# Performance work log

Measured on AMD Instinct MI355X. Metric: run time of the kernel, lower is better.

## Reference

```python
import jax, jax.numpy as jnp
import numpy as np

D_MODEL = 768
NUM_HEADS = 12
DEPTH = D_MODEL // NUM_HEADS
LN_EPS = 1e-5


def setup_inputs() -> dict:
    key = jax.random.key(0)
    ks = jax.random.split(key, 5)
    B, S = 2, 2048
    scale = 1.0 / np.sqrt(D_MODEL)
    return {
        "Q": jax.random.normal(ks[0], (B, S, D_MODEL), jnp.float32),
        "W_q": jax.random.normal(ks[1], (D_MODEL, D_MODEL), jnp.float32) * scale,
        "b_q": jnp.zeros((D_MODEL,), jnp.float32),
        "W_k": jax.random.normal(ks[2], (D_MODEL, D_MODEL), jnp.float32) * scale,
        "b_k": jnp.zeros((D_MODEL,), jnp.float32),
        "W_v": jax.random.normal(ks[3], (D_MODEL, D_MODEL), jnp.float32) * scale,
        "b_v": jnp.zeros((D_MODEL,), jnp.float32),
        "W_o": jax.random.normal(ks[4], (D_MODEL, D_MODEL), jnp.float32) * scale,
        "b_o": jnp.zeros((D_MODEL,), jnp.float32),
        "ln_gamma": jnp.ones((D_MODEL,), jnp.float32),
        "ln_beta": jnp.zeros((D_MODEL,), jnp.float32),
    }


def _split_heads(x, B):
    # [B, S, D] -> [B, H, S, depth]
    return x.reshape(B, -1, NUM_HEADS, DEPTH).transpose(0, 2, 1, 3)


def reference(Q, W_q, b_q, W_k, b_k, W_v, b_v, W_o, b_o, ln_gamma, ln_beta):
    B = Q.shape[0]
    residual = Q
    # torch Linear: x @ W.T + b
    q = _split_heads(Q @ W_q.T + b_q, B)  # [B,H,S,dh]
    k = _split_heads(Q @ W_k.T + b_k, B)
    v = _split_heads(Q @ W_v.T + b_v, B)
    scores = jnp.einsum("bhqd,bhkd->bhqk", q, k) / jnp.sqrt(jnp.float32(DEPTH))
    attn = jax.nn.softmax(scores, axis=-1)
    out = jnp.einsum("bhqk,bhkd->bhqd", attn, v)
    out = out.transpose(0, 2, 1, 3).reshape(B, -1, D_MODEL)
    out = out @ W_o.T + b_o
    x = out + residual
    mu = jnp.mean(x, axis=-1, keepdims=True)
    var = jnp.mean(jnp.square(x - mu), axis=-1, keepdims=True)
    return (x - mu) * jax.lax.rsqrt(var + LN_EPS) * ln_gamma + ln_beta
```

## Files before the change

### kernel.cpp

```cpp
#include <hip/hip_runtime.h>
#include <hip/hip_bf16.h>

#define D_MODEL 768
#define S_LEN   2048
#define BATCH   2
#define NHEAD   12
#define DH      64
#define NTOK    (BATCH * S_LEN)
#define NBH     (BATCH * NHEAD)

typedef __attribute__((ext_vector_type(8))) short bf16x8;
typedef __attribute__((ext_vector_type(4))) float f32x4;

__device__ inline unsigned short f2bf(float f) {
    union { float f; unsigned u; } v; v.f = f;
    unsigned u = v.u;
    u += 0x7fffu + ((u >> 16) & 1u);
    return (unsigned short)(u >> 16);
}

__device__ inline unsigned pack_bf2(float a, float b) {
    union { __hip_bfloat162 h2; unsigned u; } cv;
    cv.h2 = __float22bfloat162_rn(make_float2(a, b));
    return cv.u;
}

__device__ inline float bf2f(unsigned short u) {
    union { unsigned u; float f; } c; c.u = ((unsigned)u) << 16; return c.f;
}

__device__ inline void stage16(const void* g, void* l) {
    __builtin_amdgcn_global_load_lds(
        (const __attribute__((address_space(1))) unsigned*)g,
        (__attribute__((address_space(3))) unsigned*)l, 16, 0, 0);
}

__global__ __launch_bounds__(256) void convert_kernel(
    const float* __restrict__ Q,
    const float* __restrict__ Wq, const float* __restrict__ Wk,
    const float* __restrict__ Wv, const float* __restrict__ Wo,
    unsigned short* __restrict__ Xb,
    unsigned short* __restrict__ Wqb, unsigned short* __restrict__ Wkb,
    unsigned short* __restrict__ Wvb, unsigned short* __restrict__ Wob)
{
    const int XV = NTOK * D_MODEL / 4;
    const int WV = D_MODEL * D_MODEL / 4;
    int idx = blockIdx.x * 256 + threadIdx.x;
    if (idx >= XV + 4 * WV) return;

    const float* src; unsigned short* dst; int off;
    if (idx < XV) { src = Q; dst = Xb; off = idx; }
    else {
        int i2 = idx - XV;
        int seg = i2 / WV; off = i2 - seg * WV;
        if      (seg == 0) { src = Wq; dst = Wqb; }
        else if (seg == 1) { src = Wk; dst = Wkb; }
        else if (seg == 2) { src = Wv; dst = Wvb; }
        else               { src = Wo; dst = Wob; }
    }
    float4 v = reinterpret_cast<const float4*>(src)[off];
    uint2 o;
    o.x = pack_bf2(v.x, v.y);
    o.y = pack_bf2(v.z, v.w);
    reinterpret_cast<uint2*>(dst)[off] = o;
}

#define STAGE_TILE(glob, rowstrideB, row0, k0, ldsbase, nIss)                 \
    _Pragma("unroll")                                                          \
    for (int i = 0; i < (nIss); ++i) {                                         \
        int L = i * 4096 + wv * 1024 + lane * 16;                              \
        int row = L >> 7;                                                      \
        int colb = (L & 127) ^ ((row & 7) << 4);                               \
        stage16((const char*)(glob) + (size_t)((row0) + row) * (rowstrideB)    \
                    + ((k0) << 1) + colb,                                      \
                (char*)(ldsbase) + i * 4096 + wv * 1024);                      \
    }

__global__ __launch_bounds__(256) void qkv_gemm_kernel(
    const unsigned short* __restrict__ Xb,
    const unsigned short* __restrict__ Wall,
    const float* __restrict__ bq, const float* __restrict__ bk,
    const float* __restrict__ bv,
    unsigned short* __restrict__ qb, unsigned short* __restrict__ kb,
    unsigned short* __restrict__ vtb)
{
    const int lane = threadIdx.x & 63;
    const int wv   = threadIdx.x >> 6;
    const int lr   = lane & 15;
    const int lg   = lane >> 4;
    const int wr   = wv >> 1;
    const int wc   = wv & 1;
    const int row0g = blockIdx.y * 128;
    const int col0g = blockIdx.x * 128;

    __shared__ __align__(16) unsigned short At[2][128 * 64];
    __shared__ __align__(16) unsigned short Bt[2][128 * 64];

    f32x4 acc[4][4] = {};

    STAGE_TILE(Xb,   1536, row0g, 0, At[0], 4);
    STAGE_TILE(Wall, 1536, col0g, 0, Bt[0], 4);
    __syncthreads();

    for (int s = 0; s < 12; ++s) {
        int cur = s & 1;
        if (s < 11) {
            STAGE_TILE(Xb,   1536, row0g, (s + 1) * 64, At[cur ^ 1], 4);
            STAGE_TILE(Wall, 1536, col0g, (s + 1) * 64, Bt[cur ^ 1], 4);
        }
        bf16x8 a[4][2], b[4][2];
#pragma unroll
        for (int mm = 0; mm < 4; ++mm) {
            int row = wr * 64 + mm * 16 + lr, sw = (row & 7) << 4;
#pragma unroll
            for (int ks = 0; ks < 2; ++ks)
                a[mm][ks] = *reinterpret_cast<const bf16x8*>(
                    (const char*)At[cur] + row * 128 + ((ks * 64 + lg * 16) ^ sw));
        }
#pragma unroll
        for (int n = 0; n < 4; ++n) {
            int row = wc * 64 + n * 16 + lr, sw = (row & 7) << 4;
#pragma unroll
            for (int ks = 0; ks < 2; ++ks)
                b[n][ks] = *reinterpret_cast<const bf16x8*>(
                    (const char*)Bt[cur] + row * 128 + ((ks * 64 + lg * 16) ^ sw));
        }
#pragma unroll
        for (int ks = 0; ks < 2; ++ks)
#pragma unroll
            for (int mm = 0; mm < 4; ++mm)
#pragma unroll
                for (int n = 0; n < 4; ++n)
                    acc[mm][n] = __builtin_amdgcn_mfma_f32_16x16x32_bf16(
                        a[mm][ks], b[n][ks], acc[mm][n], 0, 0, 0);
        __syncthreads();
    }

    const int which   = blockIdx.x / 6;
    const int colbase = (blockIdx.x % 6) * 128;
    const float* bias = (which == 0) ? bq : (which == 1) ? bk : bv;
#pragma unroll
    for (int mm = 0; mm < 4; ++mm) {
#pragma unroll
        for (int n = 0; n < 4; ++n) {
            int col = colbase + wc * 64 + n * 16 + lr;
            float bval = bias[col];
            int h = col >> 6, d = col & 63;
            int rowg = row0g + wr * 64 + mm * 16 + lg * 4;
            int bb = rowg >> 11, s0 = rowg & 2047;
            if (which == 2) {
                uint2 w;
                w.x = pack_bf2(acc[mm][n][0] + bval, acc[mm][n][1] + bval);
                w.y = pack_bf2(acc[mm][n][2] + bval, acc[mm][n][3] + bval);
                *reinterpret_cast<uint2*>(
                    vtb + ((size_t)(bb * NHEAD + h) * DH + d) * S_LEN + s0) = w;
            } else {
                unsigned short* dst = (which == 0) ? qb : kb;
#pragma unroll
                for (int r = 0; r < 4; ++r)
                    dst[((size_t)(bb * NHEAD + h) * S_LEN + s0 + r) * DH + d] =
                        f2bf(acc[mm][n][r] + bval);
            }
        }
    }
}

#define SMPV(BUF, S, M, L, ACC, BPTR)                                          \
    {                                                                          \
        float g0 = fmaxf(fmaxf(S[0][0], S[0][1]), S[0][2]);                    \
        float g1 = fmaxf(fmaxf(S[0][3], S[1][0]), S[1][1]);                    \
        float g2 = fmaxf(fmaxf(S[1][2], S[1][3]), S[2][0]);                    \
        float g3 = fmaxf(fmaxf(S[2][1], S[2][2]), S[2][3]);                    \
        float g4 = fmaxf(fmaxf(S[3][0], S[3][1]), S[3][2]);                    \
        float mx = fmaxf(fmaxf(fmaxf(g0, g1), g2), fmaxf(fmaxf(g3, g4), S[3][3])); \
        if (__any(mx * SC > M + 8.0f)) {                                       \
            float mg = mx * SC;                                                \
            mg = fmaxf(mg, __shfl_xor(mg, 16));                                \
            mg = fmaxf(mg, __shfl_xor(mg, 32));                                \
            float mn = fmaxf(M, mg);                                           \
            float sf = __builtin_amdgcn_exp2f(M - mn);                         \
            M = mn; L *= sf;                                                   \
            _Pragma("unroll")                                                  \
            for (int t = 0; t < 4; ++t) ACC[t] *= sf;                          \
        }                                                                      \
        float p[16];                                                           \
        _Pragma("unroll")                                                      \
        for (int kt = 0; kt < 4; ++kt)                                         \
            _Pragma("unroll")                                                  \
            for (int r = 0; r < 4; ++r)                                        \
                p[kt * 4 + r] = __builtin_amdgcn_exp2f(fmaf(S[kt][r], SC, -M)); \
        float sum = ((p[0] + p[1]) + (p[2] + p[3])) + ((p[4] + p[5]) + (p[6] + p[7])); \
        sum += ((p[8] + p[9]) + (p[10] + p[11])) + ((p[12] + p[13]) + (p[14] + p[15])); \
        L += sum;                                                              \
        _Pragma("unroll")                                                      \
        for (int kt = 0; kt < 4; ++kt) {                                       \
            uint2 w;                                                           \
            w.x = pack_bf2(p[kt * 4 + 0], p[kt * 4 + 1]);                      \
            w.y = pack_bf2(p[kt * 4 + 2], p[kt * 4 + 3]);                      \
            *(uint2*)(plw + kt * 32 + lg * 8) = w;                             \
        }                                                                      \
        union { bf16x8 v; uint2 u[2]; } bp0, bp1;                              \
        bp0.u[0] = *(const uint2*)(plr);                                       \
        bp0.u[1] = *(const uint2*)(plr + 8);                                   \
        bp1.u[0] = *(const uint2*)(plr + 64);                                  \
        bp1.u[1] = *(const uint2*)(plr + 72);                                  \
        __builtin_amdgcn_s_setprio(1);                                         \
        _Pragma("unroll")                                                      \
        for (int t = 0; t < 4; ++t) {                                          \
            bf16x8 av0 = *(const bf16x8*)(rdV[BUF] + t * 2048);                \
            bf16x8 av1 = *(const bf16x8*)(rdV[BUF] + t * 2048 + oD);           \
            ACC[t] = __builtin_amdgcn_mfma_f32_16x16x32_bf16(av0, bp0.v, ACC[t], 0, 0, 0); \
            ACC[t] = __builtin_amdgcn_mfma_f32_16x16x32_bf16(av1, bp1.v, ACC[t], 0, 0, 0); \
        }                                                                      \
        __builtin_amdgcn_s_setprio(0);                                         \
    }

#define AC(BUF, DOSTAGE, VM)                                                   \
    {                                                                          \
        if (DOSTAGE) {                                                         \
            stage16(kg, sdK[((BUF) + 2) % 3]); kg += 8192;                     \
            stage16(vg, sdV[((BUF) + 2) % 3]); vg += 128;                      \
        }                                                                      \
        f32x4 sA[4] = {}, sB[4] = {};                                          \
        __builtin_amdgcn_s_setprio(1);                                         \
        _Pragma("unroll")                                                      \
        for (int kt = 0; kt < 4; ++kt) {                                       \
            bf16x8 ak0 = *(const bf16x8*)(rdK[BUF] + kt * 2048);               \
            bf16x8 ak1 = *(const bf16x8*)(rdK[BUF] + kt * 2048 + oD);          \
            sA[kt] = __builtin_amdgcn_mfma_f32_16x16x32_bf16(ak0, bqA0, sA[kt], 0, 0, 0); \
            sB[kt] = __builtin_amdgcn_mfma_f32_16x16x32_bf16(ak0, bqB0, sB[kt], 0, 0, 0); \
            sA[kt] = __builtin_amdgcn_mfma_f32_16x16x32_bf16(ak1, bqA1, sA[kt], 0, 0, 0); \
            sB[kt] = __builtin_amdgcn_mfma_f32_16x16x32_bf16(ak1, bqB1, sB[kt], 0, 0, 0); \
        }                                                                      \
        __builtin_amdgcn_s_setprio(0);                                         \
        SMPV(BUF, sA, mA, lA, accA, plr)                                       \
        SMPV(BUF, sB, mB, lB, accB, plr)                                       \
        if ((VM) == 2) {                                                       \
            asm volatile("s_waitcnt vmcnt(2)" ::: "memory");                   \
            __builtin_amdgcn_s_barrier();                                      \
        } else if ((VM) == 0) {                                                \
            asm volatile("s_waitcnt vmcnt(0)" ::: "memory");                   \
            __builtin_amdgcn_s_barrier();                                      \
        }                                                                      \
    }

template<int KS>
__global__ __launch_bounds__(512) void attn_kernel(
    const unsigned short* __restrict__ qb, const unsigned short* __restrict__ kb,
    const unsigned short* __restrict__ vtb,
    unsigned short* __restrict__ attnb,
    unsigned short* __restrict__ Opart,
    float2* __restrict__ mlbuf)
{
    const int lane = threadIdx.x & 63;
    const int wv   = threadIdx.x >> 6;
    const int lr   = lane & 15;
    const int lg   = lane >> 4;
    const int bh   = blockIdx.y;
    const int h    = bh % NHEAD, bb = bh / NHEAD;
    const int q0   = blockIdx.x * 256 + wv * 32;
    const int ks   = (KS == 2) ? blockIdx.z : 0;

    __shared__ __align__(16) unsigned short Kt[3][4096];
    __shared__ __align__(16) unsigned short Vt[3][4096];
    __shared__ __align__(16) unsigned short PL[8][16][68];

    const char* kbase = (const char*)(kb  + (size_t)bh * S_LEN * DH)
                        + (size_t)ks * (S_LEN / KS) * 128;
    const char* vbase = (const char*)(vtb + (size_t)bh * DH * S_LEN)
                        + (size_t)ks * (S_LEN / KS) * 2;
    const unsigned short* qptr = qb + ((size_t)bh * S_LEN + q0) * DH;

    bf16x8 bqA0 = *reinterpret_cast<const bf16x8*>(qptr + (size_t)lr * DH + lg * 8);
    bf16x8 bqA1 = *reinterpret_cast<const bf16x8*>(qptr + (size_t)lr * DH + 32 + lg * 8);
    bf16x8 bqB0 = *reinterpret_cast<const bf16x8*>(qptr + (size_t)(16 + lr) * DH + lg * 8);
    bf16x8 bqB1 = *reinterpret_cast<const bf16x8*>(qptr + (size_t)(16 + lr) * DH + 32 + lg * 8);

    const int swr = (lr & 7) << 4;
    const int o0  = (lg * 16) ^ swr;
    const int oD  = (o0 ^ 64) - o0;
    const int L1  = wv * 1024 + lane * 16;
    const int r1  = L1 >> 7;
    const int cb1 = (L1 & 127) ^ ((r1 & 7) << 4);

    const char* kg = kbase + (size_t)r1 * 128 + cb1;
    const char* vg = vbase + (size_t)r1 * 4096 + cb1;
    char* sdK[3] = { (char*)Kt[0] + wv * 1024, (char*)Kt[1] + wv * 1024,
                     (char*)Kt[2] + wv * 1024 };
    char* sdV[3] = { (char*)Vt[0] + wv * 1024, (char*)Vt[1] + wv * 1024,
                     (char*)Vt[2] + wv * 1024 };
    const char* rdK[3] = {
        (const char*)Kt[0] + lr * 128 + o0,
        (const char*)Kt[1] + lr * 128 + o0,
        (const char*)Kt[2] + lr * 128 + o0 };
    const char* rdV[3] = {
        (const char*)Vt[0] + lr * 128 + o0,
        (const char*)Vt[1] + lr * 128 + o0,
        (const char*)Vt[2] + lr * 128 + o0 };
    char* plw = (char*)PL + wv * 2176 + lr * 136;
    const char* plr = plw + lg * 16;

    float mA = -1e30f, lA = 0.f, mB = -1e30f, lB = 0.f;
    f32x4 accA[4] = {}, accB[4] = {};
    const float SC = 0.125f * 1.44269504088896f;

    stage16(kg, sdK[0]); kg += 8192;
    stage16(vg, sdV[0]); vg += 128;
    stage16(kg, sdK[1]); kg += 8192;
    stage16(vg, sdV[1]); vg += 128;
    asm volatile("s_waitcnt vmcnt(2)" ::: "memory");
    __builtin_amdgcn_s_barrier();

    if constexpr (KS == 2) {
        for (int it = 0; it < 4; ++it) {
            AC(0, 1, 2); AC(1, 1, 2); AC(2, 1, 2);
        }
        AC(0, 1, 2);
        AC(1, 1, 2);
        AC(2, 0, 0);
        AC(0, 0, -1);
    } else {
        for (int it = 0; it < 10; ++it) {
            AC(0, 1, 2); AC(1, 1, 2); AC(2, 1, 2);
        }
        AC(0, 0, 0);
        AC(1, 0, -1);
    }

    lA += __shfl_xor(lA, 16); lA += __shfl_xor(lA, 32);
    lB += __shfl_xor(lB, 16); lB += __shfl_xor(lB, 32);

    if constexpr (KS == 1) {
        float rlA = 1.0f / lA, rlB = 1.0f / lB;
        size_t rbA = ((size_t)(bb * S_LEN + q0 + lr)) * D_MODEL + h * DH;
        size_t rbB = ((size_t)(bb * S_LEN + q0 + 16 + lr)) * D_MODEL + h * DH;
#pragma unroll
        for (int t = 0; t < 4; ++t) {
            *reinterpret_cast<unsigned*>(attnb + rbA + t * 16 + lg * 4) =
                pack_bf2(accA[t][0] * rlA, accA[t][1] * rlA);
            *reinterpret_cast<unsigned*>(attnb + rbA + t * 16 + lg * 4 + 2) =
                pack_bf2(accA[t][2] * rlA, accA[t][3] * rlA);
            *reinterpret_cast<unsigned*>(attnb + rbB + t * 16 + lg * 4) =
                pack_bf2(accB[t][0] * rlB, accB[t][1] * rlB);
            *reinterpret_cast<unsigned*>(attnb + rbB + t * 16 + lg * 4 + 2) =
                pack_bf2(accB[t][2] * rlB, accB[t][3] * rlB);
        }
    } else {
        size_t baseA = ((size_t)(ks * NBH + bh) * S_LEN + q0 + lr) * 64;
        size_t baseB = ((size_t)(ks * NBH + bh) * S_LEN + q0 + 16 + lr) * 64;
#pragma unroll
        for (int t = 0; t < 4; ++t) {
            *reinterpret_cast<unsigned*>(Opart + baseA + t * 16 + lg * 4) =
                pack_bf2(accA[t][0], accA[t][1]);
            *reinterpret_cast<unsigned*>(Opart + baseA + t * 16 + lg * 4 + 2) =
                pack_bf2(accA[t][2], accA[t][3]);
            *reinterpret_cast<unsigned*>(Opart + baseB + t * 16 + lg * 4) =
                pack_bf2(accB[t][0], accB[t][1]);
            *reinterpret_cast<unsigned*>(Opart + baseB + t * 16 + lg * 4 + 2) =
                pack_bf2(accB[t][2], accB[t][3]);
        }
        if (lg == 0) {
            mlbuf[(size_t)(ks * NBH + bh) * S_LEN + q0 + lr]      = make_float2(mA, lA);
            mlbuf[(size_t)(ks * NBH + bh) * S_LEN + q0 + 16 + lr] = make_float2(mB, lB);
        }
    }
}

__global__ __launch_bounds__(256) void combine_kernel(
    const unsigned short* __restrict__ Opart,
    const float2* __restrict__ mlbuf,
    unsigned short* __restrict__ attnb)
{
    int idx = blockIdx.x * 256 + threadIdx.x;
    int d4  = idx & 15;
    int h   = (idx >> 4) % 12;
    int tok = idx / 192;
    int bb  = tok >> 11, s = tok & 2047;
    size_t qoff = (size_t)(bb * NHEAD + h) * S_LEN + s;

    float2 ml0 = mlbuf[qoff];
    float2 ml1 = mlbuf[(size_t)NBH * S_LEN + qoff];
    float M  = fmaxf(ml0.x, ml1.x);
    float w0 = __builtin_amdgcn_exp2f(ml0.x - M);
    float w1 = __builtin_amdgcn_exp2f(ml1.x - M);
    float ri = 1.0f / (w0 * ml0.y + w1 * ml1.y);
    w0 *= ri; w1 *= ri;

    size_t ob = qoff * 64 + d4 * 4;
    ushort4 a = *reinterpret_cast<const ushort4*>(Opart + ob);
    ushort4 b = *reinterpret_cast<const ushort4*>(Opart + (size_t)NBH * S_LEN * 64 + ob);
    float o0 = bf2f(a.x) * w0 + bf2f(b.x) * w1;
    float o1 = bf2f(a.y) * w0 + bf2f(b.y) * w1;
    float o2 = bf2f(a.z) * w0 + bf2f(b.z) * w1;
    float o3 = bf2f(a.w) * w0 + bf2f(b.w) * w1;
    uint2 w;
    w.x = pack_bf2(o0, o1);
    w.y = pack_bf2(o2, o3);
    *reinterpret_cast<uint2*>(attnb + (size_t)tok * D_MODEL + h * 64 + d4 * 4) = w;
}

__global__ __launch_bounds__(256) void oproj_kernel(
    const unsigned short* __restrict__ attnb, const unsigned short* __restrict__ Wob,
    const float* __restrict__ bo, const float* __restrict__ Qres,
    float* __restrict__ Y)
{
    const int lane = threadIdx.x & 63;
    const int wv   = threadIdx.x >> 6;
    const int lr   = lane & 15;
    const int lg   = lane >> 4;
    const int row0g = blockIdx.y * 128;
    const int col0g = blockIdx.x * 64;

    __shared__ __align__(16) unsigned short At[2][128 * 64];
    __shared__ __align__(16) unsigned short Bt[2][64 * 64];

    f32x4 acc[2][4] = {};

    STAGE_TILE(attnb, 1536, row0g, 0, At[0], 4);
    STAGE_TILE(Wob,   1536, col0g, 0, Bt[0], 2);
    __syncthreads();

    for (int s = 0; s < 12; ++s) {
        int cur = s & 1;
        if (s < 11) {
            STAGE_TILE(attnb, 1536, row0g, (s + 1) * 64, At[cur ^ 1], 4);
            STAGE_TILE(Wob,   1536, col0g, (s + 1) * 64, Bt[cur ^ 1], 2);
        }
        bf16x8 a[2][2], b[4][2];
#pragma unroll
        for (int mm = 0; mm < 2; ++mm) {
            int row = wv * 32 + mm * 16 + lr, sw = (row & 7) << 4;
#pragma unroll
            for (int ks = 0; ks < 2; ++ks)
                a[mm][ks] = *reinterpret_cast<const bf16x8*>(
                    (const char*)At[cur] + row * 128 + ((ks * 64 + lg * 16) ^ sw));
        }
#pragma unroll
        for (int n = 0; n < 4; ++n) {
            int row = n * 16 + lr, sw = (row & 7) << 4;
#pragma unroll
            for (int ks = 0; ks < 2; ++ks)
                b[n][ks] = *reinterpret_cast<const bf16x8*>(
                    (const char*)Bt[cur] + row * 128 + ((ks * 64 + lg * 16) ^ sw));
        }
#pragma unroll
        for (int ks = 0; ks < 2; ++ks)
#pragma unroll
            for (int mm = 0; mm < 2; ++mm)
#pragma unroll
                for (int n = 0; n < 4; ++n)
                    acc[mm][n] = __builtin_amdgcn_mfma_f32_16x16x32_bf16(
                        a[mm][ks], b[n][ks], acc[mm][n], 0, 0, 0);
        __syncthreads();
    }

#pragma unroll
    for (int mm = 0; mm < 2; ++mm)
#pragma unroll
        for (int n = 0; n < 4; ++n) {
            int col = col0g + n * 16 + lr;
            float bval = bo[col];
#pragma unroll
            for (int r = 0; r < 4; ++r) {
                int row = row0g + wv * 32 + mm * 16 + lg * 4 + r;
                size_t off = (size_t)row * D_MODEL + col;
                Y[off] = acc[mm][n][r] + bval + Qres[off];
            }
        }
}

__global__ __launch_bounds__(256) void ln_kernel(
    const float* __restrict__ Y,
    const float* __restrict__ gamma, const float* __restrict__ beta,
    float* __restrict__ out)
{
    const int lane = threadIdx.x & 63;
    const int row  = blockIdx.x * 4 + (threadIdx.x >> 6);
    const float4* yr = reinterpret_cast<const float4*>(Y + (size_t)row * D_MODEL);

    float4 v[3];
    float sum = 0.f, ss = 0.f;
#pragma unroll
    for (int j = 0; j < 3; ++j) {
        v[j] = yr[lane + 64 * j];
        sum += v[j].x + v[j].y + v[j].z + v[j].w;
        ss  += v[j].x * v[j].x + v[j].y * v[j].y + v[j].z * v[j].z + v[j].w * v[j].w;
    }
#pragma unroll
    for (int msk = 1; msk < 64; msk <<= 1) {
        sum += __shfl_xor(sum, msk);
        ss  += __shfl_xor(ss,  msk);
    }
    float mu  = sum * (1.f / 768.f);
    float var = ss * (1.f / 768.f) - mu * mu;
    float is  = rsqrtf(var + 1e-5f);

    const float4* g4 = reinterpret_cast<const float4*>(gamma);
    const float4* b4 = reinterpret_cast<const float4*>(beta);
    float4* o4 = reinterpret_cast<float4*>(out + (size_t)row * D_MODEL);
#pragma unroll
    for (int j = 0; j < 3; ++j) {
        float4 g = g4[lane + 64 * j], b = b4[lane + 64 * j], r;
        r.x = (v[j].x - mu) * is * g.x + b.x;
        r.y = (v[j].y - mu) * is * g.y + b.y;
        r.z = (v[j].z - mu) * is * g.z + b.z;
        r.w = (v[j].w - mu) * is * g.w + b.w;
        o4[lane + 64 * j] = r;
    }
}

extern "C" void kernel_launch(void* const* d_in, const int* in_sizes, int n_in,
                              void* d_out, int out_size, void* d_ws, size_t ws_size,
                              hipStream_t stream)
{
    const float* Q     = (const float*)d_in[0];
    const float* Wq    = (const float*)d_in[1];
    const float* bq    = (const float*)d_in[2];
    const float* Wk    = (const float*)d_in[3];
    const float* bk    = (const float*)d_in[4];
    const float* Wv    = (const float*)d_in[5];
    const float* bv    = (const float*)d_in[6];
    const float* Wo    = (const float*)d_in[7];
    const float* bo    = (const float*)d_in[8];
    const float* gamma = (const float*)d_in[9];
    const float* beta  = (const float*)d_in[10];
    float* out = (float*)d_out;

    char* ws = (char*)d_ws;
    unsigned short* Xb    = (unsigned short*)(ws + 0);
    unsigned short* Wqb   = (unsigned short*)(ws + 6291456);
    unsigned short* Wkb   = (unsigned short*)(ws + 7471104);
    unsigned short* Wvb   = (unsigned short*)(ws + 8650752);
    unsigned short* Wob   = (unsigned short*)(ws + 9830400);
    unsigned short* qb    = (unsigned short*)(ws + 11010048);
    unsigned short* kb    = (unsigned short*)(ws + 17301504);
    unsigned short* vtb   = (unsigned short*)(ws + 23592960);
    unsigned short* attnb = (unsigned short*)(ws + 29884416);
    float*          Yf    = (float*)        (ws + 36175872);
    unsigned short* Opartb = (unsigned short*)(ws + 36175872);
    float2*         mlbuf  = (float2*)       (ws + 61341696);

    const bool splitk = (ws_size >= 62128128ull);

    convert_kernel<<<5376, 256, 0, stream>>>(Q, Wq, Wk, Wv, Wo, Xb, Wqb, Wkb, Wvb, Wob);
    qkv_gemm_kernel<<<dim3(18, 32), 256, 0, stream>>>(Xb, Wqb, bq, bk, bv, qb, kb, vtb);
    if (splitk) {
        attn_kernel<2><<<dim3(8, 24, 2), 512, 0, stream>>>(qb, kb, vtb, attnb,
                                                           Opartb, mlbuf);
        combine_kernel<<<3072, 256, 0, stream>>>(Opartb, mlbuf, attnb);
    } else {
        attn_kernel<1><<<dim3(8, 24), 512, 0, stream>>>(qb, kb, vtb, attnb,
                                                        Opartb, mlbuf);
    }
    oproj_kernel<<<dim3(12, 32), 256, 0, stream>>>(attnb, Wob, bo, Q, Yf);
    ln_kernel<<<1024, 256, 0, stream>>>(Yf, gamma, beta, out);
}
```

Before: 128.6 us.

## Remap blocks per XCD and shrink attention blocks to 256 threads with double buffering

```diff
diff --git a/kernel.cpp b/kernel.cpp
--- a/kernel.cpp
+++ b/kernel.cpp
@@ -90,8 +90,14 @@
     const int lg   = lane >> 4;
     const int wr   = wv >> 1;
     const int wc   = wv & 1;
-    const int row0g = blockIdx.y * 128;
-    const int col0g = blockIdx.x * 128;
+
+    const int flat = blockIdx.x + 18 * blockIdx.y;
+    const int xcd  = flat & 7;
+    const int j    = flat >> 3;
+    const int ybt  = xcd * 4 + j / 18;
+    const int xbt  = j % 18;
+    const int row0g = ybt * 128;
+    const int col0g = xbt * 128;
 
     __shared__ __align__(16) unsigned short At[2][128 * 64];
     __shared__ __align__(16) unsigned short Bt[2][128 * 64];
@@ -136,8 +142,8 @@
         __syncthreads();
     }
 
-    const int which   = blockIdx.x / 6;
-    const int colbase = (blockIdx.x % 6) * 128;
+    const int which   = xbt / 6;
+    const int colbase = (xbt % 6) * 128;
     const float* bias = (which == 0) ? bq : (which == 1) ? bk : bv;
 #pragma unroll
     for (int mm = 0; mm < 4; ++mm) {
@@ -165,7 +171,7 @@
     }
 }
 
-#define SMPV(BUF, S, M, L, ACC, BPTR)                                          \
+#define SMPV(S, M, L, ACC)                                                     \
     {                                                                          \
         float g0 = fmaxf(fmaxf(S[0][0], S[0][1]), S[0][2]);                    \
         float g1 = fmaxf(fmaxf(S[0][3], S[1][0]), S[1][1]);                    \
@@ -207,45 +213,44 @@
         __builtin_amdgcn_s_setprio(1);                                         \
         _Pragma("unroll")                                                      \
         for (int t = 0; t < 4; ++t) {                                          \
-            bf16x8 av0 = *(const bf16x8*)(rdV[BUF] + t * 2048);                \
-            bf16x8 av1 = *(const bf16x8*)(rdV[BUF] + t * 2048 + oD);           \
-            ACC[t] = __builtin_amdgcn_mfma_f32_16x16x32_bf16(av0, bp0.v, ACC[t], 0, 0, 0); \
-            ACC[t] = __builtin_amdgcn_mfma_f32_16x16x32_bf16(av1, bp1.v, ACC[t], 0, 0, 0); \
+            ACC[t] = __builtin_amdgcn_mfma_f32_16x16x32_bf16(av0[t], bp0.v, ACC[t], 0, 0, 0); \
+            ACC[t] = __builtin_amdgcn_mfma_f32_16x16x32_bf16(av1[t], bp1.v, ACC[t], 0, 0, 0); \
         }                                                                      \
         __builtin_amdgcn_s_setprio(0);                                         \
     }
 
-#define AC(BUF, DOSTAGE, VM)                                                   \
+#define AC(CUR, DOSTAGE, DOBAR)                                                \
     {                                                                          \
         if (DOSTAGE) {                                                         \
-            stage16(kg, sdK[((BUF) + 2) % 3]); kg += 8192;                     \
-            stage16(vg, sdV[((BUF) + 2) % 3]); vg += 128;                      \
+            stage16(kg0, sdK[(CUR) ^ 1]); stage16(kg1, sdK[(CUR) ^ 1] + 1024); \
+            stage16(vg0, sdV[(CUR) ^ 1]); stage16(vg1, sdV[(CUR) ^ 1] + 1024); \
+            kg0 += 8192; kg1 += 8192; vg0 += 128; vg1 += 128;                  \
         }                                                                      \
         f32x4 sA[4] = {}, sB[4] = {};                                          \
         __builtin_amdgcn_s_setprio(1);                                         \
         _Pragma("unroll")                                                      \
         for (int kt = 0; kt < 4; ++kt) {                                       \
-            bf16x8 ak0 = *(const bf16x8*)(rdK[BUF] + kt * 2048);               \
-            bf16x8 ak1 = *(const bf16x8*)(rdK[BUF] + kt * 2048 + oD);          \
+            bf16x8 ak0 = *(const bf16x8*)(rdK[CUR] + kt * 2048);               \
+            bf16x8 ak1 = *(const bf16x8*)(rdK[CUR] + kt * 2048 + oD);          \
             sA[kt] = __builtin_amdgcn_mfma_f32_16x16x32_bf16(ak0, bqA0, sA[kt], 0, 0, 0); \
             sB[kt] = __builtin_amdgcn_mfma_f32_16x16x32_bf16(ak0, bqB0, sB[kt], 0, 0, 0); \
             sA[kt] = __builtin_amdgcn_mfma_f32_16x16x32_bf16(ak1, bqA1, sA[kt], 0, 0, 0); \
             sB[kt] = __builtin_amdgcn_mfma_f32_16x16x32_bf16(ak1, bqB1, sB[kt], 0, 0, 0); \
         }                                                                      \
         __builtin_amdgcn_s_setprio(0);                                         \
-        SMPV(BUF, sA, mA, lA, accA, plr)                                       \
-        SMPV(BUF, sB, mB, lB, accB, plr)                                       \
-        if ((VM) == 2) {                                                       \
-            asm volatile("s_waitcnt vmcnt(2)" ::: "memory");                   \
-            __builtin_amdgcn_s_barrier();                                      \
-        } else if ((VM) == 0) {                                                \
-            asm volatile("s_waitcnt vmcnt(0)" ::: "memory");                   \
-            __builtin_amdgcn_s_barrier();                                      \
+        bf16x8 av0[4], av1[4];                                                 \
+        _Pragma("unroll")                                                      \
+        for (int t = 0; t < 4; ++t) {                                          \
+            av0[t] = *(const bf16x8*)(rdV[CUR] + t * 2048);                    \
+            av1[t] = *(const bf16x8*)(rdV[CUR] + t * 2048 + oD);               \
         }                                                                      \
+        SMPV(sA, mA, lA, accA)                                                 \
+        SMPV(sB, mB, lB, accB)                                                 \
+        if (DOBAR) __syncthreads();                                            \
     }
 
 template<int KS>
-__global__ __launch_bounds__(512) void attn_kernel(
+__global__ __launch_bounds__(256) void attn_kernel(
     const unsigned short* __restrict__ qb, const unsigned short* __restrict__ kb,
     const unsigned short* __restrict__ vtb,
     unsigned short* __restrict__ attnb,
@@ -256,14 +261,20 @@
     const int wv   = threadIdx.x >> 6;
     const int lr   = lane & 15;
     const int lg   = lane >> 4;
-    const int bh   = blockIdx.y;
-    const int h    = bh % NHEAD, bb = bh / NHEAD;
-    const int q0   = blockIdx.x * 256 + wv * 32;
-    const int ks   = (KS == 2) ? blockIdx.z : 0;
-
-    __shared__ __align__(16) unsigned short Kt[3][4096];
-    __shared__ __align__(16) unsigned short Vt[3][4096];
-    __shared__ __align__(16) unsigned short PL[8][16][68];
+
+    int flat = blockIdx.x + 16 * blockIdx.y + ((KS == 2) ? 384 * blockIdx.z : 0);
+    const int xcd = flat & 7;
+    const int j   = flat >> 3;
+    const int g   = xcd * ((KS == 2) ? 6 : 3) + (j >> 4);
+    const int qt  = j & 15;
+    const int bh  = (KS == 2) ? (g % 24) : g;
+    const int ks  = (KS == 2) ? (g / 24) : 0;
+    const int h   = bh % NHEAD, bb = bh / NHEAD;
+    const int q0  = qt * 128 + wv * 32;
+
+    __shared__ __align__(16) unsigned short Kt[2][4096];
+    __shared__ __align__(16) unsigned short Vt[2][4096];
+    __shared__ __align__(16) unsigned short PL[4][16][68];
 
     const char* kbase = (const char*)(kb  + (size_t)bh * S_LEN * DH)
                         + (size_t)ks * (S_LEN / KS) * 128;
@@ -279,24 +290,25 @@
     const int swr = (lr & 7) << 4;
     const int o0  = (lg * 16) ^ swr;
     const int oD  = (o0 ^ 64) - o0;
-    const int L1  = wv * 1024 + lane * 16;
+    const int L0  = wv * 2048 + lane * 16;
+    const int r0  = L0 >> 7;
+    const int cb0 = (L0 & 127) ^ ((r0 & 7) << 4);
+    const int L1  = L0 + 1024;
     const int r1  = L1 >> 7;
     const int cb1 = (L1 & 127) ^ ((r1 & 7) << 4);
 
-    const char* kg = kbase + (size_t)r1 * 128 + cb1;
-    const char* vg = vbase + (size_t)r1 * 4096 + cb1;
-    char* sdK[3] = { (char*)Kt[0] + wv * 1024, (char*)Kt[1] + wv * 1024,
-                     (char*)Kt[2] + wv * 1024 };
-    char* sdV[3] = { (char*)Vt[0] + wv * 1024, (char*)Vt[1] + wv * 1024,
-                     (char*)Vt[2] + wv * 1024 };
-    const char* rdK[3] = {
+    const char* kg0 = kbase + (size_t)r0 * 128 + cb0;
+    const char* kg1 = kbase + (size_t)r1 * 128 + cb1;
+    const char* vg0 = vbase + (size_t)r0 * 4096 + cb0;
+    const char* vg1 = vbase + (size_t)r1 * 4096 + cb1;
+    char* sdK[2] = { (char*)Kt[0] + wv * 2048, (char*)Kt[1] + wv * 2048 };
+    char* sdV[2] = { (char*)Vt[0] + wv * 2048, (char*)Vt[1] + wv * 2048 };
+    const char* rdK[2] = {
         (const char*)Kt[0] + lr * 128 + o0,
-        (const char*)Kt[1] + lr * 128 + o0,
-        (const char*)Kt[2] + lr * 128 + o0 };
-    const char* rdV[3] = {
+        (const char*)Kt[1] + lr * 128 + o0 };
+    const char* rdV[2] = {
         (const char*)Vt[0] + lr * 128 + o0,
-        (const char*)Vt[1] + lr * 128 + o0,
-        (const char*)Vt[2] + lr * 128 + o0 };
+        (const char*)Vt[1] + lr * 128 + o0 };
     char* plw = (char*)PL + wv * 2176 + lr * 136;
     const char* plr = plw + lg * 16;
 
@@ -304,27 +316,19 @@
     f32x4 accA[4] = {}, accB[4] = {};
     const float SC = 0.125f * 1.44269504088896f;
 
-    stage16(kg, sdK[0]); kg += 8192;
-    stage16(vg, sdV[0]); vg += 128;
-    stage16(kg, sdK[1]); kg += 8192;
-    stage16(vg, sdV[1]); vg += 128;
-    asm volatile("s_waitcnt vmcnt(2)" ::: "memory");
-    __builtin_amdgcn_s_barrier();
+    stage16(kg0, sdK[0]); stage16(kg1, sdK[0] + 1024);
+    stage16(vg0, sdV[0]); stage16(vg1, sdV[0] + 1024);
+    kg0 += 8192; kg1 += 8192; vg0 += 128; vg1 += 128;
+    __syncthreads();
 
     if constexpr (KS == 2) {
-        for (int it = 0; it < 4; ++it) {
-            AC(0, 1, 2); AC(1, 1, 2); AC(2, 1, 2);
-        }
-        AC(0, 1, 2);
-        AC(1, 1, 2);
-        AC(2, 0, 0);
-        AC(0, 0, -1);
+        for (int it = 0; it < 7; ++it) { AC(0, 1, 1); AC(1, 1, 1); }
+        AC(0, 1, 1);
+        AC(1, 0, 0);
     } else {
-        for (int it = 0; it < 10; ++it) {
-            AC(0, 1, 2); AC(1, 1, 2); AC(2, 1, 2);
-        }
-        AC(0, 0, 0);
-        AC(1, 0, -1);
+        for (int it = 0; it < 15; ++it) { AC(0, 1, 1); AC(1, 1, 1); }
+        AC(0, 1, 1);
+        AC(1, 0, 0);
     }
 
     lA += __shfl_xor(lA, 16); lA += __shfl_xor(lA, 32);
@@ -408,8 +412,14 @@
     const int wv   = threadIdx.x >> 6;
     const int lr   = lane & 15;
     const int lg   = lane >> 4;
-    const int row0g = blockIdx.y * 128;
-    const int col0g = blockIdx.x * 64;
+
+    const int flat = blockIdx.x + 12 * blockIdx.y;
+    const int xcd  = flat & 7;
+    const int j    = flat >> 3;
+    const int ybt  = xcd * 4 + j / 12;
+    const int xbt  = j % 12;
+    const int row0g = ybt * 128;
+    const int col0g = xbt * 64;
 
     __shared__ __align__(16) unsigned short At[2][128 * 64];
     __shared__ __align__(16) unsigned short Bt[2][64 * 64];
@@ -545,12 +555,12 @@
     convert_kernel<<<5376, 256, 0, stream>>>(Q, Wq, Wk, Wv, Wo, Xb, Wqb, Wkb, Wvb, Wob);
     qkv_gemm_kernel<<<dim3(18, 32), 256, 0, stream>>>(Xb, Wqb, bq, bk, bv, qb, kb, vtb);
     if (splitk) {
-        attn_kernel<2><<<dim3(8, 24, 2), 512, 0, stream>>>(qb, kb, vtb, attnb,
-                                                           Opartb, mlbuf);
+        attn_kernel<2><<<dim3(16, 24, 2), 256, 0, stream>>>(qb, kb, vtb, attnb,
+                                                            Opartb, mlbuf);
         combine_kernel<<<3072, 256, 0, stream>>>(Opartb, mlbuf, attnb);
     } else {
-        attn_kernel<1><<<dim3(8, 24), 512, 0, stream>>>(qb, kb, vtb, attnb,
-                                                        Opartb, mlbuf);
+        attn_kernel<1><<<dim3(16, 24), 256, 0, stream>>>(qb, kb, vtb, attnb,
+                                                         Opartb, mlbuf);
     }
     oproj_kernel<<<dim3(12, 32), 256, 0, stream>>>(attnb, Wob, bo, Q, Yf);
     ln_kernel<<<1024, 256, 0, stream>>>(Yf, gamma, beta, out);
```

New measurement: 118.1 us. 8.2% less time.
